# Optimization experiments

Hardware: AMD Instinct MI355X
Metric: run time of the kernel (lower is better)

The kernel has to match this reference:

```python
import jax, jax.numpy as jnp
import numpy as np

B, S, D, H = 4, 2048, 512, 8
DK = D // H


def setup_inputs() -> dict:
    key = jax.random.key(0)
    ks = jax.random.split(key, 12)
    s = 0.02
    return {
        "q": jax.random.normal(ks[0], (B, S, D), jnp.float32),
        "k": jax.random.normal(ks[1], (B, S, D), jnp.float32),
        "v": jax.random.normal(ks[2], (B, S, D), jnp.float32),
        "mask": jax.random.randint(ks[3], (B, 1, S, S), 0, 2, jnp.int32),
        "Wq": jax.random.normal(ks[4], (D, D), jnp.float32) * s,
        "bq": jnp.zeros((D,), jnp.float32),
        "Wk": jax.random.normal(ks[5], (D, D), jnp.float32) * s,
        "bk": jnp.zeros((D,), jnp.float32),
        "Wv": jax.random.normal(ks[6], (D, D), jnp.float32) * s,
        "bv": jnp.zeros((D,), jnp.float32),
        "Wo": jax.random.normal(ks[7], (D, D), jnp.float32) * s,
        "bo": jnp.zeros((D,), jnp.float32),
    }


def reference(q, k, v, mask, Wq, bq, Wk, bk, Wv, bv, Wo, bo):
    # Linear projections (torch Linear: x @ W.T + b)
    qh = (q @ Wq.T + bq).reshape(B, S, H, DK).transpose(0, 2, 1, 3)  # [B,H,S,dk]
    kh = (k @ Wk.T + bk).reshape(B, S, H, DK).transpose(0, 2, 1, 3)
    vh = (v @ Wv.T + bv).reshape(B, S, H, DK).transpose(0, 2, 1, 3)
    # FAITHFUL quirk: original divides by q.shape[1] AFTER transpose == num_heads
    scores = jnp.einsum("bhqd,bhkd->bhqk", qh, kh) / H  # [B,H,S,S]
    scores = jnp.where(mask == 0, jnp.float32(-1e9), scores)
    attn = jax.nn.softmax(scores, axis=-1)
    ctx = jnp.einsum("bhqk,bhkd->bhqd", attn, vh)  # [B,H,S,dk]
    x = ctx.transpose(0, 2, 1, 3).reshape(B, S, D)
    return x @ Wo.T + bo  # dropout is identity in eval mode
```

## Files before the change

### kernel.cpp

```cpp
#include <hip/hip_runtime.h>
#include <math.h>

constexpr int Bc  = 4;
constexpr int Sc  = 2048;
constexpr int Dc  = 512;
constexpr int Hc  = 8;
constexpr int DKc = 64;
constexpr int Mc  = Bc * Sc;

constexpr float SCALE_Q = 0.180336880111120426f;

typedef __attribute__((ext_vector_type(8)))  short s16x8;
typedef __attribute__((ext_vector_type(4)))  float f32x4;
typedef __attribute__((ext_vector_type(16))) float f32x16;

__device__ __forceinline__ unsigned short f2bf(float f) {
    __bf16 h = (__bf16)f;
    return __builtin_bit_cast(unsigned short, h);
}

__device__ __forceinline__ float fexp2(float x) {
#if __has_builtin(__builtin_amdgcn_exp2f)
    return __builtin_amdgcn_exp2f(x);
#else
    return __expf(x * 0.6931471805599453f);
#endif
}

__global__ __launch_bounds__(256)
void pack_mask(const int* __restrict__ mask, unsigned long long* __restrict__ out,
               int nwords)
{
    int gw   = (blockIdx.x * blockDim.x + threadIdx.x) >> 6;
    int lane = threadIdx.x & 63;
    int nw   = (gridDim.x * blockDim.x) >> 6;
    for (int w0 = gw * 4; w0 < nwords; w0 += nw * 4) {
        int vals[4];
#pragma unroll
        for (int c = 0; c < 4; ++c)
            vals[c] = mask[(size_t)(w0 + c) * 64 + lane];
#pragma unroll
        for (int c = 0; c < 4; ++c) {
            unsigned long long bits = __ballot(vals[c] != 0);
            if (lane == 0) out[w0 + c] = bits;
        }
    }
}

__global__ __launch_bounds__(256)
void cvt4(const float* __restrict__ i0, const float* __restrict__ i1,
          const float* __restrict__ i2, const float* __restrict__ i3,
          unsigned short* __restrict__ o0, unsigned short* __restrict__ o1,
          unsigned short* __restrict__ o2, unsigned short* __restrict__ o3,
          int n4)
{
    const float* in; unsigned short* out;
    switch (blockIdx.y) {
        case 0: in = i0; out = o0; break;
        case 1: in = i1; out = o1; break;
        case 2: in = i2; out = o2; break;
        default: in = i3; out = o3; break;
    }
    int i = blockIdx.x * 256 + threadIdx.x;
    if (i < n4) {
        float4 v = ((const float4*)in)[i];
        ushort4 r;
        r.x = f2bf(v.x); r.y = f2bf(v.y); r.z = f2bf(v.z); r.w = f2bf(v.w);
        ((ushort4*)out)[i] = r;
    }
}

__global__ __launch_bounds__(256, 3)
void gemm128(const unsigned short* __restrict__ x0, const unsigned short* __restrict__ x1,
             const unsigned short* __restrict__ x2,
             const unsigned short* __restrict__ w0, const unsigned short* __restrict__ w1,
             const unsigned short* __restrict__ w2,
             const float* __restrict__ b0, const float* __restrict__ b1,
             const float* __restrict__ b2,
             void* __restrict__ o0v, void* __restrict__ o1v, void* __restrict__ o2v,
             float s0, float s1, float s2, int m0, int m1, int m2)
{
    const unsigned short* X; const unsigned short* W; const float* bias; void* outv;
    float scale; int mode;
    switch (blockIdx.z) {
        case 0:  X = x0; W = w0; bias = b0; outv = o0v; scale = s0; mode = m0; break;
        case 1:  X = x1; W = w1; bias = b1; outv = o1v; scale = s1; mode = m1; break;
        default: X = x2; W = w2; bias = b2; outv = o2v; scale = s2; mode = m2; break;
    }

    __shared__ unsigned short Xs[2][128 * 64];
    __shared__ unsigned short Ws[2][64 * 64];

    const int tid = threadIdx.x;
    const int w = tid >> 6, lane = tid & 63, ln = lane & 15, qd = lane >> 4;
    const int wm = (w >> 1) * 64, wn = (w & 1) * 32;
    const int row0 = blockIdx.x * 128, col0 = blockIdx.y * 64;

    f32x4 acc[4][2];
#pragma unroll
    for (int mt = 0; mt < 4; ++mt)
#pragma unroll
        for (int nt = 0; nt < 2; ++nt) acc[mt][nt] = f32x4{0.f, 0.f, 0.f, 0.f};

    auto stage = [&](int buf, int k0) {
#pragma unroll
        for (int c = 0; c < 4; ++c) {
            const int s = c * 256 + w * 64 + lane;
            const int r = s >> 3, cc = (s & 7) ^ (r & 7);
            const unsigned short* gs = X + (size_t)(row0 + r) * 512 + k0 + cc * 8;
            __builtin_amdgcn_global_load_lds(
                (const __attribute__((address_space(1))) unsigned int*)gs,
                (__attribute__((address_space(3))) unsigned int*)
                    ((char*)&Xs[buf][0] + (c * 256 + w * 64) * 16),
                16, 0, 0);
        }
#pragma unroll
        for (int c = 0; c < 2; ++c) {
            const int s = c * 256 + w * 64 + lane;
            const int r = s >> 3, cc = (s & 7) ^ (r & 7);
            const unsigned short* gs = W + (size_t)(col0 + r) * 512 + k0 + cc * 8;
            __builtin_amdgcn_global_load_lds(
                (const __attribute__((address_space(1))) unsigned int*)gs,
                (__attribute__((address_space(3))) unsigned int*)
                    ((char*)&Ws[buf][0] + (c * 256 + w * 64) * 16),
                16, 0, 0);
        }
    };

    stage(0, 0);
    for (int k0 = 0; k0 < 512; k0 += 64) {
        const int buf = (k0 >> 6) & 1;
        __syncthreads();
        if (k0 + 64 < 512) stage(buf ^ 1, k0 + 64);
#pragma unroll
        for (int kc = 0; kc < 2; ++kc) {
            s16x8 af[4], bfr[2];
#pragma unroll
            for (int mt = 0; mt < 4; ++mt) {
                int r = wm + mt * 16 + ln;
                af[mt] = *(const s16x8*)&Xs[buf][r * 64 + (((kc * 4 + qd) ^ (ln & 7)) * 8)];
            }
#pragma unroll
            for (int nt = 0; nt < 2; ++nt) {
                int r = wn + nt * 16 + ln;
                bfr[nt] = *(const s16x8*)&Ws[buf][r * 64 + (((kc * 4 + qd) ^ (ln & 7)) * 8)];
            }
#pragma unroll
            for (int mt = 0; mt < 4; ++mt)
#pragma unroll
                for (int nt = 0; nt < 2; ++nt)
                    acc[mt][nt] = __builtin_amdgcn_mfma_f32_16x16x32_bf16(
                        af[mt], bfr[nt], acc[mt][nt], 0, 0, 0);
        }
    }

    if (mode == 0) {
#pragma unroll
        for (int nt = 0; nt < 2; ++nt) {
            const int n = col0 + wn + nt * 16 + ln;
            const float bz = bias[n];
#pragma unroll
            for (int mt = 0; mt < 4; ++mt) {
                const int mbase = row0 + wm + mt * 16 + qd * 4;
                float* o = (float*)outv;
#pragma unroll
                for (int r = 0; r < 4; ++r)
                    o[(size_t)(mbase + r) * 512 + n] = acc[mt][nt][r] + bz;
            }
        }
    } else if (mode == 1) {
        __syncthreads();
        unsigned short* T = &Xs[0][0];
#pragma unroll
        for (int nt = 0; nt < 2; ++nt) {
            const int n = col0 + wn + nt * 16 + ln;
            const float bz = bias[n];
            const int dk = n & 63;
#pragma unroll
            for (int mt = 0; mt < 4; ++mt) {
                const int ml = wm + mt * 16 + qd * 4;
#pragma unroll
                for (int r = 0; r < 4; ++r)
                    T[(ml + r) * 72 + dk] = f2bf((acc[mt][nt][r] + bz) * scale);
            }
        }
        __syncthreads();
        const int sl = tid >> 1, halfo = (tid & 1) * 32;
        const int h = col0 >> 6, bb = row0 >> 11, sm = row0 & 2047;
        const unsigned short* Tr = &T[sl * 72 + halfo];
        uint4 d0 = *(const uint4*)(Tr);
        uint4 d1 = *(const uint4*)(Tr + 8);
        uint4 d2 = *(const uint4*)(Tr + 16);
        uint4 d3 = *(const uint4*)(Tr + 24);
        unsigned short* o = (unsigned short*)outv +
                            ((size_t)(bb * Hc + h) * Sc + sm + sl) * 64 + halfo;
        *(uint4*)(o)      = d0;
        *(uint4*)(o + 8)  = d1;
        *(uint4*)(o + 16) = d2;
        *(uint4*)(o + 24) = d3;
    } else {
        __syncthreads();
        unsigned short* T2 = &Xs[0][0];
#pragma unroll
        for (int nt = 0; nt < 2; ++nt) {
            const int n = col0 + wn + nt * 16 + ln;
            const float bz = bias[n];
            const int dk = n & 63;
#pragma unroll
            for (int mt = 0; mt < 4; ++mt) {
                const int ml = wm + mt * 16 + qd * 4;
                const int sw = (ml & ~12) | ((ml & 4) << 1) | ((ml & 8) >> 1);
#pragma unroll
                for (int r = 0; r < 4; ++r)
                    T2[dk * 136 + sw + r] = f2bf((acc[mt][nt][r] + bz) * scale);
            }
        }
        __syncthreads();
        const int dv = tid >> 2, qo = (tid & 3) * 32;
        const int h = col0 >> 6, bb = row0 >> 11, sm = row0 & 2047;
        const unsigned short* Tr = &T2[dv * 136 + qo];
        uint4 d0 = *(const uint4*)(Tr);
        uint4 d1 = *(const uint4*)(Tr + 8);
        uint4 d2 = *(const uint4*)(Tr + 16);
        uint4 d3 = *(const uint4*)(Tr + 24);
        unsigned short* o = (unsigned short*)outv +
                            ((size_t)(bb * Hc + h) * 64 + dv) * Sc + sm + qo;
        *(uint4*)(o)      = d0;
        *(uint4*)(o + 8)  = d1;
        *(uint4*)(o + 16) = d2;
        *(uint4*)(o + 24) = d3;
    }
}

__global__ __launch_bounds__(256, 4)
void attn_mfma(const unsigned short* __restrict__ qh, const unsigned short* __restrict__ kh,
               const unsigned short* __restrict__ vt, const unsigned* __restrict__ mbits,
               unsigned short* __restrict__ ctx)
{
    __shared__ uint4 smem4[2][1024];

    const int pwg = blockIdx.y * gridDim.x + blockIdx.x;
    const int lg  = (pwg & 7) * 128 + (pwg >> 3);
    const int bh = lg >> 5, b = bh >> 3, h = bh & 7;
    const int q0 = (lg & 31) * 64;

    const int tid = threadIdx.x;
    const int w = tid >> 6;
    const int g = w >> 1;
    const int kh_ = w & 1;
    const int lane = tid & 63, ln = lane & 31, hf = lane >> 5;
    const int wv = tid >> 7;
    const int qr = q0 + g * 32 + ln;

    s16x8 qf[4];
    {
        const unsigned short* qp = qh + ((size_t)bh * Sc + qr) * 64 + hf * 8;
#pragma unroll
        for (int kc = 0; kc < 4; ++kc)
            qf[kc] = *(const s16x8*)(qp + kc * 16);
    }

    f32x16 o0, o1;
#pragma unroll
    for (int r = 0; r < 16; ++r) { o0[r] = 0.f; o1[r] = 0.f; }
    float lr = 0.f;

    const unsigned* mr = mbits + ((size_t)b * Sc + qr) * (Sc / 32);
    const unsigned short* kbase = kh + (size_t)bh * Sc * 64;
    const unsigned short* vbase = vt + (size_t)bh * 64 * Sc;

    const int kt0 = kh_ * 1024;

    auto stage_tile = [&](int buf, int kt) {
        char* gb = (char*)smem4[buf] + kh_ * 8192;
#pragma unroll
        for (int c = 0; c < 2; ++c) {
            const int seg = wv * 2 + c;
            const int s   = seg * 64 + lane;
            const int r   = s >> 3, cc = (s & 7) ^ (r & 7);
            const unsigned short* gs = kbase + (size_t)(kt + r) * 64 + cc * 8;
            __builtin_amdgcn_global_load_lds(
                (const __attribute__((address_space(1))) unsigned int*)gs,
                (__attribute__((address_space(3))) unsigned int*)(gb + seg * 1024),
                16, 0, 0);
        }
        char* vb = gb + 4096;
#pragma unroll
        for (int c = 0; c < 2; ++c) {
            const int seg = wv * 2 + c;
            const int dv  = lane ^ (seg << 1);
            const unsigned short* gs = vbase + (size_t)dv * Sc + kt + seg * 8;
            __builtin_amdgcn_global_load_lds(
                (const __attribute__((address_space(1))) unsigned int*)gs,
                (__attribute__((address_space(3))) unsigned int*)(vb + seg * 1024),
                16, 0, 0);
        }
    };

    stage_tile(0, kt0);
    unsigned mwn = mr[kt0 >> 5];

    for (int i = 0; i < 32; ++i) {
        const int kt = kt0 + i * 32;
        const int buf = i & 1;
        __syncthreads();
        const unsigned mw = mwn;
        if (i < 31) {
            stage_tile(buf ^ 1, kt + 32);
            mwn = mr[(kt + 32) >> 5];
        }

        const unsigned short* Ks = (const unsigned short*)smem4[buf] + kh_ * 4096;
        const unsigned short* Vs = Ks + 2048;

        f32x16 sv;
#pragma unroll
        for (int r = 0; r < 16; ++r) sv[r] = 0.f;
        __builtin_amdgcn_s_setprio(1);
#pragma unroll
        for (int kc = 0; kc < 4; ++kc) {
            s16x8 kf = *(const s16x8*)&Ks[ln * 64 + ((((kc << 1) | hf) ^ (ln & 7)) * 8)];
            sv = __builtin_amdgcn_mfma_f32_32x32x16_bf16(kf, qf[kc], sv, 0, 0, 0);
        }
        __builtin_amdgcn_s_setprio(0);

        float ps = 0.f;
        unsigned pu[8];
#pragma unroll
        for (int r = 0; r < 16; r += 2) {
            int key0 = (r & 3) + 8 * (r >> 2) + 4 * hf;
            int key1 = ((r + 1) & 3) + 8 * ((r + 1) >> 2) + 4 * hf;
            float a0 = ((mw >> key0) & 1u) ? sv[r]     : -1e9f;
            float a1 = ((mw >> key1) & 1u) ? sv[r + 1] : -1e9f;
            float p0 = fexp2(a0), p1 = fexp2(a1);
            ps += p0 + p1;
            pu[r >> 1] = (unsigned)f2bf(p0) | ((unsigned)f2bf(p1) << 16);
        }
        lr += ps;

        __builtin_amdgcn_s_setprio(1);
#pragma unroll
        for (int kc = 0; kc < 2; ++kc) {
            uint4 ua; ua.x = pu[4*kc]; ua.y = pu[4*kc+1]; ua.z = pu[4*kc+2]; ua.w = pu[4*kc+3];
            s16x8 pf = __builtin_bit_cast(s16x8, ua);
            const int cc = (kc << 1) | hf;
            s16x8 v0  = *(const s16x8*)&Vs[(cc * 64 + (ln ^ (cc << 1))) * 8];
            s16x8 v1  = *(const s16x8*)&Vs[(cc * 64 + ((32 + ln) ^ (cc << 1))) * 8];
            o0 = __builtin_amdgcn_mfma_f32_32x32x16_bf16(v0, pf, o0, 0, 0, 0);
            o1 = __builtin_amdgcn_mfma_f32_32x32x16_bf16(v1, pf, o1, 0, 0, 0);
        }
        __builtin_amdgcn_s_setprio(0);
    }

    lr += __shfl_xor(lr, 32);

    __syncthreads();
    float* cs = (float*)smem4[0];
    const int row = g * 64 + lane;
    float* my = cs + (size_t)row * 48;
    const int sw = lane & 7;
    if (kh_ == 1) {
#pragma unroll
        for (int r = 0; r < 4; ++r) {
            *(float4*)(my + ((r ^ sw) * 4))       = make_float4(o0[4*r], o0[4*r+1], o0[4*r+2], o0[4*r+3]);
            *(float4*)(my + (((r + 4) ^ sw) * 4)) = make_float4(o1[4*r], o1[4*r+1], o1[4*r+2], o1[4*r+3]);
        }
        my[32] = lr;
    }
    __syncthreads();
    if (kh_ == 0) {
        lr += my[32];
        const float inv = 1.f / lr;
#pragma unroll
        for (int r = 0; r < 4; ++r) {
            float4 a0 = *(const float4*)(my + ((r ^ sw) * 4));
            float4 a1 = *(const float4*)(my + (((r + 4) ^ sw) * 4));
            o0[4*r]   = (o0[4*r]   + a0.x) * inv; o0[4*r+1] = (o0[4*r+1] + a0.y) * inv;
            o0[4*r+2] = (o0[4*r+2] + a0.z) * inv; o0[4*r+3] = (o0[4*r+3] + a0.w) * inv;
            o1[4*r]   = (o1[4*r]   + a1.x) * inv; o1[4*r+1] = (o1[4*r+1] + a1.y) * inv;
            o1[4*r+2] = (o1[4*r+2] + a1.z) * inv; o1[4*r+3] = (o1[4*r+3] + a1.w) * inv;
        }
        unsigned short* op = ctx + ((size_t)(b * Sc + qr)) * 512 + h * 64;
#pragma unroll
        for (int gg = 0; gg < 4; ++gg) {
            ushort4 a, c;
            a.x = f2bf(o0[gg*4+0]); a.y = f2bf(o0[gg*4+1]);
            a.z = f2bf(o0[gg*4+2]); a.w = f2bf(o0[gg*4+3]);
            c.x = f2bf(o1[gg*4+0]); c.y = f2bf(o1[gg*4+1]);
            c.z = f2bf(o1[gg*4+2]); c.w = f2bf(o1[gg*4+3]);
            *(ushort4*)(op + 8 * gg + 4 * hf)      = a;
            *(ushort4*)(op + 32 + 8 * gg + 4 * hf) = c;
        }
    }
}

extern "C" void kernel_launch(void* const* d_in, const int* in_sizes, int n_in,
                              void* d_out, int out_size, void* d_ws, size_t ws_size,
                              hipStream_t stream)
{
    (void)in_sizes; (void)n_in; (void)out_size; (void)ws_size;

    const float* q    = (const float*)d_in[0];
    const float* k    = (const float*)d_in[1];
    const float* v    = (const float*)d_in[2];
    const int*   mask = (const int*)  d_in[3];
    const float* Wq   = (const float*)d_in[4];
    const float* bq   = (const float*)d_in[5];
    const float* Wk   = (const float*)d_in[6];
    const float* bk   = (const float*)d_in[7];
    const float* Wv   = (const float*)d_in[8];
    const float* bv   = (const float*)d_in[9];
    const float* Wo   = (const float*)d_in[10];
    const float* bo   = (const float*)d_in[11];
    float* out = (float*)d_out;

    constexpr size_t TEN = (size_t)Bc * Hc * Sc * DKc;
    char* p = (char*)d_ws;
    unsigned short* wqb   = (unsigned short*)p;  p += (size_t)Dc * Dc * 2;
    unsigned short* wkb   = (unsigned short*)p;  p += (size_t)Dc * Dc * 2;
    unsigned short* wvb   = (unsigned short*)p;  p += (size_t)Dc * Dc * 2;
    unsigned short* wob   = (unsigned short*)p;  p += (size_t)Dc * Dc * 2;
    unsigned short* qh_bf = (unsigned short*)p;  p += TEN * 2;
    unsigned short* kh_bf = (unsigned short*)p;  p += TEN * 2;
    unsigned short* vt_bf = (unsigned short*)p;  p += TEN * 2;
    unsigned short* ctx   = (unsigned short*)p;  p += TEN * 2;
    unsigned long long* mb64 = (unsigned long long*)p;

    unsigned short* qb = (unsigned short*)d_out;
    unsigned short* kb = qb + TEN;
    unsigned short* vb = ctx;

    const int nwords = Bc * Sc * (Sc / 64);

    dim3 bb(256);

    pack_mask<<<dim3(16384), bb, 0, stream>>>(mask, mb64, nwords);
    cvt4<<<dim3(Dc * Dc / 4 / 256, 4), bb, 0, stream>>>(Wq, Wk, Wv, Wo, wqb, wkb, wvb, wob,
                                                        Dc * Dc / 4);
    cvt4<<<dim3((int)(TEN / 4 / 256), 3), bb, 0, stream>>>(q, k, v, v, qb, kb, vb, vb,
                                                           (int)(TEN / 4));
    gemm128<<<dim3(Mc / 128, Dc / 64, 3), bb, 0, stream>>>(
        qb, kb, vb, wqb, wkb, wvb, bq, bk, bv, qh_bf, kh_bf, vt_bf,
        SCALE_Q, 1.0f, 1.0f, 1, 1, 2);
    attn_mfma<<<dim3(Sc / 64, Bc * Hc), bb, 0, stream>>>(qh_bf, kh_bf, vt_bf,
                                                         (const unsigned*)mb64, ctx);
    gemm128<<<dim3(Mc / 128, Dc / 64, 1), bb, 0, stream>>>(
        ctx, ctx, ctx, wob, wob, wob, bo, bo, bo, out, out, out,
        1.0f, 1.0f, 1.0f, 0, 0, 0);
}
```

Baseline: 265.7 us.

## Merge prep kernels and transpose packed mask for coalesced LDS staging

Folds the mask bit-packing and the two bf16 conversion launches into one prep kernel, removing two kernel launches. The packed mask is now written transposed (key-word major, query contiguous), so the attention kernel can stage each tile's mask words into LDS with a coalesced async global-to-LDS load alongside K/V instead of issuing a strided per-lane global load. The mask packing now reads 64 rows per wave with a strided pattern and goes through a shared-memory transpose, which may make mask reads less efficient in prep.

```diff
diff --git a/kernel.cpp b/kernel.cpp
--- a/kernel.cpp
+++ b/kernel.cpp
@@ -28,45 +28,62 @@
 }
 
 __global__ __launch_bounds__(256)
-void pack_mask(const int* __restrict__ mask, unsigned long long* __restrict__ out,
-               int nwords)
+void prep(const float* __restrict__ Wq, const float* __restrict__ Wk,
+          const float* __restrict__ Wv, const float* __restrict__ Wo,
+          unsigned short* __restrict__ wqb, unsigned short* __restrict__ wkb,
+          unsigned short* __restrict__ wvb, unsigned short* __restrict__ wob,
+          const float* __restrict__ q, const float* __restrict__ k,
+          const float* __restrict__ v,
+          unsigned short* __restrict__ qb, unsigned short* __restrict__ kb,
+          unsigned short* __restrict__ vb,
+          const int* __restrict__ mask, unsigned* __restrict__ mbT)
 {
-    int gw   = (blockIdx.x * blockDim.x + threadIdx.x) >> 6;
-    int lane = threadIdx.x & 63;
-    int nw   = (gridDim.x * blockDim.x) >> 6;
-    for (int w0 = gw * 4; w0 < nwords; w0 += nw * 4) {
-        int vals[4];
-#pragma unroll
-        for (int c = 0; c < 4; ++c)
-            vals[c] = mask[(size_t)(w0 + c) * 64 + lane];
-#pragma unroll
-        for (int c = 0; c < 4; ++c) {
-            unsigned long long bits = __ballot(vals[c] != 0);
-            if (lane == 0) out[w0 + c] = bits;
-        }
-    }
-}
-
-__global__ __launch_bounds__(256)
-void cvt4(const float* __restrict__ i0, const float* __restrict__ i1,
-          const float* __restrict__ i2, const float* __restrict__ i3,
-          unsigned short* __restrict__ o0, unsigned short* __restrict__ o1,
-          unsigned short* __restrict__ o2, unsigned short* __restrict__ o3,
-          int n4)
-{
-    const float* in; unsigned short* out;
-    switch (blockIdx.y) {
-        case 0: in = i0; out = o0; break;
-        case 1: in = i1; out = o1; break;
-        case 2: in = i2; out = o2; break;
-        default: in = i3; out = o3; break;
-    }
-    int i = blockIdx.x * 256 + threadIdx.x;
-    if (i < n4) {
-        float4 v = ((const float4*)in)[i];
+    const int blk = blockIdx.x, tid = threadIdx.x;
+    if (blk < 1024) {
+        const int idx = blk * 256 + tid;
+        const int t = idx >> 16, i = idx & 65535;
+        const float* in; unsigned short* out;
+        switch (t) {
+            case 0: in = Wq; out = wqb; break;
+            case 1: in = Wk; out = wkb; break;
+            case 2: in = Wv; out = wvb; break;
+            default: in = Wo; out = wob; break;
+        }
+        float4 f = ((const float4*)in)[i];
         ushort4 r;
-        r.x = f2bf(v.x); r.y = f2bf(v.y); r.z = f2bf(v.z); r.w = f2bf(v.w);
+        r.x = f2bf(f.x); r.y = f2bf(f.y); r.z = f2bf(f.z); r.w = f2bf(f.w);
         ((ushort4*)out)[i] = r;
+    } else if (blk < 13312) {
+        const int idx = (blk - 1024) * 256 + tid;
+        const int t = idx >> 20, i = idx & 1048575;
+        const float* in; unsigned short* out;
+        switch (t) {
+            case 0: in = q; out = qb; break;
+            case 1: in = k; out = kb; break;
+            default: in = v; out = vb; break;
+        }
+        float4 f = ((const float4*)in)[i];
+        ushort4 r;
+        r.x = f2bf(f.x); r.y = f2bf(f.y); r.z = f2bf(f.z); r.w = f2bf(f.w);
+        ((ushort4*)out)[i] = r;
+    } else {
+        __shared__ unsigned long long pl[4][64];
+        const int wv = tid >> 6, lane = tid & 63;
+        const int wid = (blk - 13312) * 4 + wv;
+        const int b = wid >> 10, rest = wid & 1023;
+        const int qb0 = (rest >> 5) * 64, w64 = rest & 31;
+        const int* mrow = mask + ((size_t)b * Sc + qb0) * Sc + w64 * 64 + lane;
+#pragma unroll 4
+        for (int qq = 0; qq < 64; ++qq) {
+            unsigned long long bits = __ballot(mrow[(size_t)qq * Sc] != 0);
+            if (lane == 0) pl[wv][qq] = bits;
+        }
+        __builtin_amdgcn_s_waitcnt(0);
+        unsigned long long wbits = pl[wv][lane];
+        unsigned* o_lo = mbT + ((size_t)(b * 64) + w64 * 2) * Sc + qb0;
+        unsigned* o_hi = o_lo + Sc;
+        o_lo[lane] = (unsigned)wbits;
+        o_hi[lane] = (unsigned)(wbits >> 32);
     }
 }
 
@@ -234,10 +251,11 @@
 
 __global__ __launch_bounds__(256, 4)
 void attn_mfma(const unsigned short* __restrict__ qh, const unsigned short* __restrict__ kh,
-               const unsigned short* __restrict__ vt, const unsigned* __restrict__ mbits,
+               const unsigned short* __restrict__ vt, const unsigned* __restrict__ mbT,
                unsigned short* __restrict__ ctx)
 {
     __shared__ uint4 smem4[2][1024];
+    __shared__ unsigned mstage[2][2][64];
 
     const int pwg = blockIdx.y * gridDim.x + blockIdx.x;
     const int lg  = (pwg & 7) * 128 + (pwg >> 3);
@@ -265,9 +283,9 @@
     for (int r = 0; r < 16; ++r) { o0[r] = 0.f; o1[r] = 0.f; }
     float lr = 0.f;
 
-    const unsigned* mr = mbits + ((size_t)b * Sc + qr) * (Sc / 32);
     const unsigned short* kbase = kh + (size_t)bh * Sc * 64;
     const unsigned short* vbase = vt + (size_t)bh * 64 * Sc;
+    const unsigned* mbase = mbT + (size_t)(b * 64) * Sc + q0;
 
     const int kt0 = kh_ * 1024;
 
@@ -295,20 +313,24 @@
                 (__attribute__((address_space(3))) unsigned int*)(vb + seg * 1024),
                 16, 0, 0);
         }
+        if (wv == 0) {
+            const unsigned* ms = mbase + (size_t)(kt >> 5) * Sc + lane;
+            __builtin_amdgcn_global_load_lds(
+                (const __attribute__((address_space(1))) unsigned int*)ms,
+                (__attribute__((address_space(3))) unsigned int*)&mstage[buf][kh_][0],
+                4, 0, 0);
+        }
     };
 
     stage_tile(0, kt0);
-    unsigned mwn = mr[kt0 >> 5];
 
     for (int i = 0; i < 32; ++i) {
         const int kt = kt0 + i * 32;
         const int buf = i & 1;
         __syncthreads();
-        const unsigned mw = mwn;
-        if (i < 31) {
-            stage_tile(buf ^ 1, kt + 32);
-            mwn = mr[(kt + 32) >> 5];
-        }
+        if (i < 31) stage_tile(buf ^ 1, kt + 32);
+
+        const unsigned mw = mstage[buf][kh_][g * 32 + ln];
 
         const unsigned short* Ks = (const unsigned short*)smem4[buf] + kh_ * 4096;
         const unsigned short* Vs = Ks + 2048;
@@ -424,26 +446,21 @@
     unsigned short* kh_bf = (unsigned short*)p;  p += TEN * 2;
     unsigned short* vt_bf = (unsigned short*)p;  p += TEN * 2;
     unsigned short* ctx   = (unsigned short*)p;  p += TEN * 2;
-    unsigned long long* mb64 = (unsigned long long*)p;
+    unsigned* mbT = (unsigned*)p;
 
     unsigned short* qb = (unsigned short*)d_out;
     unsigned short* kb = qb + TEN;
     unsigned short* vb = ctx;
 
-    const int nwords = Bc * Sc * (Sc / 64);
-
     dim3 bb(256);
 
-    pack_mask<<<dim3(16384), bb, 0, stream>>>(mask, mb64, nwords);
-    cvt4<<<dim3(Dc * Dc / 4 / 256, 4), bb, 0, stream>>>(Wq, Wk, Wv, Wo, wqb, wkb, wvb, wob,
-                                                        Dc * Dc / 4);
-    cvt4<<<dim3((int)(TEN / 4 / 256), 3), bb, 0, stream>>>(q, k, v, v, qb, kb, vb, vb,
-                                                           (int)(TEN / 4));
+    prep<<<dim3(14336), bb, 0, stream>>>(Wq, Wk, Wv, Wo, wqb, wkb, wvb, wob,
+                                         q, k, v, qb, kb, vb, mask, mbT);
     gemm128<<<dim3(Mc / 128, Dc / 64, 3), bb, 0, stream>>>(
         qb, kb, vb, wqb, wkb, wvb, bq, bk, bv, qh_bf, kh_bf, vt_bf,
         SCALE_Q, 1.0f, 1.0f, 1, 1, 2);
     attn_mfma<<<dim3(Sc / 64, Bc * Hc), bb, 0, stream>>>(qh_bf, kh_bf, vt_bf,
-                                                         (const unsigned*)mb64, ctx);
+                                                         mbT, ctx);
     gemm128<<<dim3(Mc / 128, Dc / 64, 1), bb, 0, stream>>>(
         ctx, ctx, ctx, wob, wob, wob, bo, bo, bo, out, out, out,
         1.0f, 1.0f, 1.0f, 0, 0, 0);
```

After: 284.3 us. +7.0%, slower.

## Transpose packed mask layout and stage mask words into LDS with async loads

Applied to the files above, without the earlier changes.

The mask-packing kernel now writes 32-bit mask words in a key-block-major, query-contiguous layout, so each key tile's mask words for a 64-query block are contiguous. The attention kernel fetches these words with global_load_lds into a small double-buffered LDS stage alongside the K/V tiles. This replaces the strided per-lane global load, which ran one row of 2048/32 words apart per query. The cost is an extra LDS buffer, an LDS read per iteration, and a packing kernel that does 16 ballots per wave with lane selects.

```diff
diff --git a/kernel.cpp b/kernel.cpp
--- a/kernel.cpp
+++ b/kernel.cpp
@@ -28,22 +28,25 @@
 }
 
 __global__ __launch_bounds__(256)
-void pack_mask(const int* __restrict__ mask, unsigned long long* __restrict__ out,
-               int nwords)
+void pack_maskT(const int* __restrict__ mask, unsigned* __restrict__ mbT)
 {
-    int gw   = (blockIdx.x * blockDim.x + threadIdx.x) >> 6;
-    int lane = threadIdx.x & 63;
-    int nw   = (gridDim.x * blockDim.x) >> 6;
-    for (int w0 = gw * 4; w0 < nwords; w0 += nw * 4) {
-        int vals[4];
-#pragma unroll
-        for (int c = 0; c < 4; ++c)
-            vals[c] = mask[(size_t)(w0 + c) * 64 + lane];
-#pragma unroll
-        for (int c = 0; c < 4; ++c) {
-            unsigned long long bits = __ballot(vals[c] != 0);
-            if (lane == 0) out[w0 + c] = bits;
-        }
+    const int wv = threadIdx.x >> 6, lane = threadIdx.x & 63;
+    const int wid = blockIdx.x * 4 + wv;
+    const int job = wid >> 2, part = wid & 3;
+    const int b = job >> 10, rest = job & 1023;
+    const int qb0 = (rest >> 5) * 64, w64 = rest & 31;
+    const int* mrow = mask + ((size_t)(b * Sc + qb0 + part * 16)) * Sc + w64 * 64 + lane;
+    unsigned wsel = 0;
+#pragma unroll
+    for (int qq = 0; qq < 16; ++qq) {
+        unsigned long long bits = __ballot(mrow[(size_t)qq * Sc] != 0);
+        wsel = (lane == qq)      ? (unsigned)bits         : wsel;
+        wsel = (lane == qq + 16) ? (unsigned)(bits >> 32) : wsel;
+    }
+    if (lane < 32) {
+        unsigned* orow = mbT + ((size_t)(b * 64 + w64 * 2 + (lane >> 4))) * Sc
+                             + qb0 + part * 16 + (lane & 15);
+        *orow = wsel;
     }
 }
 
@@ -234,10 +237,11 @@
 
 __global__ __launch_bounds__(256, 4)
 void attn_mfma(const unsigned short* __restrict__ qh, const unsigned short* __restrict__ kh,
-               const unsigned short* __restrict__ vt, const unsigned* __restrict__ mbits,
+               const unsigned short* __restrict__ vt, const unsigned* __restrict__ mbT,
                unsigned short* __restrict__ ctx)
 {
     __shared__ uint4 smem4[2][1024];
+    __shared__ unsigned mstage[2][2][64];
 
     const int pwg = blockIdx.y * gridDim.x + blockIdx.x;
     const int lg  = (pwg & 7) * 128 + (pwg >> 3);
@@ -265,9 +269,9 @@
     for (int r = 0; r < 16; ++r) { o0[r] = 0.f; o1[r] = 0.f; }
     float lr = 0.f;
 
-    const unsigned* mr = mbits + ((size_t)b * Sc + qr) * (Sc / 32);
     const unsigned short* kbase = kh + (size_t)bh * Sc * 64;
     const unsigned short* vbase = vt + (size_t)bh * 64 * Sc;
+    const unsigned* mbase = mbT + (size_t)(b * 64) * Sc + q0;
 
     const int kt0 = kh_ * 1024;
 
@@ -295,20 +299,24 @@
                 (__attribute__((address_space(3))) unsigned int*)(vb + seg * 1024),
                 16, 0, 0);
         }
+        if (wv == 0) {
+            const unsigned* ms = mbase + (size_t)(kt >> 5) * Sc + lane;
+            __builtin_amdgcn_global_load_lds(
+                (const __attribute__((address_space(1))) unsigned int*)ms,
+                (__attribute__((address_space(3))) unsigned int*)&mstage[buf][kh_][0],
+                4, 0, 0);
+        }
     };
 
     stage_tile(0, kt0);
-    unsigned mwn = mr[kt0 >> 5];
 
     for (int i = 0; i < 32; ++i) {
         const int kt = kt0 + i * 32;
         const int buf = i & 1;
         __syncthreads();
-        const unsigned mw = mwn;
-        if (i < 31) {
-            stage_tile(buf ^ 1, kt + 32);
-            mwn = mr[(kt + 32) >> 5];
-        }
+        if (i < 31) stage_tile(buf ^ 1, kt + 32);
+
+        const unsigned mw = mstage[buf][kh_][g * 32 + ln];
 
         const unsigned short* Ks = (const unsigned short*)smem4[buf] + kh_ * 4096;
         const unsigned short* Vs = Ks + 2048;
@@ -424,17 +432,15 @@
     unsigned short* kh_bf = (unsigned short*)p;  p += TEN * 2;
     unsigned short* vt_bf = (unsigned short*)p;  p += TEN * 2;
     unsigned short* ctx   = (unsigned short*)p;  p += TEN * 2;
-    unsigned long long* mb64 = (unsigned long long*)p;
+    unsigned* mbT = (unsigned*)p;
 
     unsigned short* qb = (unsigned short*)d_out;
     unsigned short* kb = qb + TEN;
     unsigned short* vb = ctx;
 
-    const int nwords = Bc * Sc * (Sc / 64);
-
     dim3 bb(256);
 
-    pack_mask<<<dim3(16384), bb, 0, stream>>>(mask, mb64, nwords);
+    pack_maskT<<<dim3(4096), bb, 0, stream>>>(mask, mbT);
     cvt4<<<dim3(Dc * Dc / 4 / 256, 4), bb, 0, stream>>>(Wq, Wk, Wv, Wo, wqb, wkb, wvb, wob,
                                                         Dc * Dc / 4);
     cvt4<<<dim3((int)(TEN / 4 / 256), 3), bb, 0, stream>>>(q, k, v, v, qb, kb, vb, vb,
@@ -443,7 +449,7 @@
         qb, kb, vb, wqb, wkb, wvb, bq, bk, bv, qh_bf, kh_bf, vt_bf,
         SCALE_Q, 1.0f, 1.0f, 1, 1, 2);
     attn_mfma<<<dim3(Sc / 64, Bc * Hc), bb, 0, stream>>>(qh_bf, kh_bf, vt_bf,
-                                                         (const unsigned*)mb64, ctx);
+                                                         mbT, ctx);
     gemm128<<<dim3(Mc / 128, Dc / 64, 1), bb, 0, stream>>>(
         ctx, ctx, ctx, wob, wob, wob, bo, bo, bo, out, out, out,
         1.0f, 1.0f, 1.0f, 0, 0, 0);
```

After: 269.7 us. About the same (+1.5%).
